# Performance work log

Hardware: AMD Instinct MI355X
Metric: run time of the kernel (lower is better)

The kernel has to match this reference:

```python
import math
import jax, jax.numpy as jnp
import numpy as np

NH, NKV, HD, THETA = 32, 8, 128, 500000.0

def rotate_half(x):
    x1, x2 = jnp.split(x, 2, axis=-1)
    return jnp.concatenate((-x2, x1), axis=-1)

def rope_cos_sin(seq_len, dim, base, dtype):
    inv_freq = 1.0 / (base ** (jnp.arange(0, dim, 2, dtype=jnp.float32) / dim))
    t = jnp.arange(seq_len, dtype=jnp.float32)
    freqs = jnp.outer(t, inv_freq)              # [S, dim/2]
    emb = jnp.concatenate((freqs, freqs), -1)   # [S, dim]
    return jnp.cos(emb).astype(dtype), jnp.sin(emb).astype(dtype)

def setup_inputs() -> dict:
    key = jax.random.key(0)
    ks = jax.random.split(key, 5)
    B, S, H = 1, 2048, 4096
    sc = 1.0 / math.sqrt(H)
    return {
        'x':  jax.random.normal(ks[0], (B, S, H), jnp.float32),
        'wq': jax.random.normal(ks[1], (H, H), jnp.float32) * sc,
        'wk': jax.random.normal(ks[2], (NKV * HD, H), jnp.float32) * sc,
        'wv': jax.random.normal(ks[3], (NKV * HD, H), jnp.float32) * sc,
        'wo': jax.random.normal(ks[4], (H, H), jnp.float32) * sc,
    }

def attention(x, wq, wk, wv, wo):
    B, S, H = x.shape
    n_rep = NH // NKV
    q = (x @ wq.T).reshape(B, S, NH, HD).transpose(0, 2, 1, 3)    # [B,NH,S,HD]
    k = (x @ wk.T).reshape(B, S, NKV, HD).transpose(0, 2, 1, 3)   # [B,NKV,S,HD]
    v = (x @ wv.T).reshape(B, S, NKV, HD).transpose(0, 2, 1, 3)
    cos, sin = rope_cos_sin(S, HD, THETA, x.dtype)                # [S,HD]
    cos = cos[None, None]; sin = sin[None, None]
    q = q * cos + rotate_half(q) * sin
    k = k * cos + rotate_half(k) * sin
    k = jnp.repeat(k, n_rep, axis=1)                               # [B,NH,S,HD]
    v = jnp.repeat(v, n_rep, axis=1)
    scores = jnp.einsum('bhqd,bhkd->bhqk', q, k) / math.sqrt(HD)
    causal = jnp.tril(jnp.ones((S, S), dtype=bool))
    scores = jnp.where(causal, scores, jnp.finfo(scores.dtype).min)
    probs = jax.nn.softmax(scores, axis=-1)
    out = jnp.einsum('bhqk,bhkd->bhqd', probs, v)                  # [B,NH,S,HD]
    out = out.transpose(0, 2, 1, 3).reshape(B, S, H)
    return out @ wo.T

def reference(x, wq, wk, wv, wo):
    return attention(x, wq, wk, wv, wo)
```

## Files before the change

### kernel.cpp

```cpp
#include <hip/hip_runtime.h>
#include <hip/hip_bf16.h>
#include <math.h>

typedef __bf16 bf16x8 __attribute__((ext_vector_type(8)));
typedef __bf16 bf16x4 __attribute__((ext_vector_type(4)));
typedef unsigned short u16x8 __attribute__((ext_vector_type(8)));
typedef float  f32x4  __attribute__((ext_vector_type(4)));

constexpr int kS   = 2048;
constexpr int kH   = 4096;
constexpr int kNH  = 32;
constexpr int kNKV = 8;
constexpr int kHD  = 128;
constexpr int kQKV = kH + 2 * kNKV * kHD;
constexpr int kKOff = kH;
constexpr int kVOff = kH + kNKV * kHD;

__global__ void cast_bf16(const float* __restrict__ in, __bf16* __restrict__ out, int n4) {
    int i = blockIdx.x * blockDim.x + threadIdx.x;
    if (i < n4) {
        float4 f = ((const float4*)in)[i];
        bf16x4 o;
        o[0] = (__bf16)f.x; o[1] = (__bf16)f.y; o[2] = (__bf16)f.z; o[3] = (__bf16)f.w;
        ((bf16x4*)out)[i] = o;
    }
}

__global__ void cast_all(const float* __restrict__ x, const float* __restrict__ wq,
                         const float* __restrict__ wk, const float* __restrict__ wv,
                         __bf16* __restrict__ xb, __bf16* __restrict__ wqkv) {
    int i = blockIdx.x * 256 + threadIdx.x;
    float4 f;
    __bf16* dst;
    int di;
    if (i < (1 << 21)) {
        f = ((const float4*)x)[i];
        dst = xb; di = i;
    } else {
        int j = i - (1 << 21);
        const float4* s = (j < (1 << 22)) ? ((const float4*)wq + j)
                        : (j < (5 << 20)) ? ((const float4*)wk + (j - (1 << 22)))
                                          : ((const float4*)wv + (j - (5 << 20)));
        f = *s;
        dst = wqkv; di = j;
    }
    bf16x4 o;
    o[0] = (__bf16)f.x; o[1] = (__bf16)f.y; o[2] = (__bf16)f.z; o[3] = (__bf16)f.w;
    ((bf16x4*)dst)[di] = o;
}

constexpr int BM = 128, BN = 128, BK = 32;

__device__ inline void gld16(const __bf16* g, __bf16* l) {
    __builtin_amdgcn_global_load_lds((const __attribute__((address_space(1))) void*)g,
                                     (__attribute__((address_space(3))) void*)l, 16, 0, 0);
}

template <typename OutT>
__global__ __launch_bounds__(256) void gemm_nt(const __bf16* __restrict__ A,
                                               const __bf16* __restrict__ B,
                                               OutT* __restrict__ C,
                                               int M, int N, int K) {
    __shared__ __align__(16) __bf16 As[BM * BK];
    __shared__ __align__(16) __bf16 Bs[BN * BK];
    const int tid  = threadIdx.x;
    const int w    = tid >> 6, lane = tid & 63;
    const int m0   = blockIdx.y * BM, n0 = blockIdx.x * BN;
    const int wm   = (w >> 1) * 64, wn = (w & 1) * 64;
    const int lr   = lane & 15, lk = (lane >> 4) * 8;

    const int ci0 = w * 128 + lane;
    const int ci1 = ci0 + 64;
    const __bf16* gA0 = A + (size_t)(m0 + (ci0 >> 2)) * K + (ci0 & 3) * 8;
    const __bf16* gA1 = A + (size_t)(m0 + (ci1 >> 2)) * K + (ci1 & 3) * 8;
    const __bf16* gB0 = B + (size_t)(n0 + (ci0 >> 2)) * K + (ci0 & 3) * 8;
    const __bf16* gB1 = B + (size_t)(n0 + (ci1 >> 2)) * K + (ci1 & 3) * 8;
    __bf16* lA0 = As + w * 1024;
    __bf16* lA1 = As + w * 1024 + 512;
    __bf16* lB0 = Bs + w * 1024;
    __bf16* lB1 = Bs + w * 1024 + 512;

    f32x4 acc[4][4];
#pragma unroll
    for (int i = 0; i < 4; i++)
#pragma unroll
        for (int j = 0; j < 4; j++) acc[i][j] = (f32x4)(0.f);

    for (int k0 = 0; k0 < K; k0 += BK) {
        gld16(gA0 + k0, lA0);
        gld16(gA1 + k0, lA1);
        gld16(gB0 + k0, lB0);
        gld16(gB1 + k0, lB1);
        __syncthreads();

        bf16x8 af[4], bfr[4];
#pragma unroll
        for (int i = 0; i < 4; i++) af[i]  = *(const bf16x8*)&As[(wm + i * 16 + lr) * BK + lk];
#pragma unroll
        for (int j = 0; j < 4; j++) bfr[j] = *(const bf16x8*)&Bs[(wn + j * 16 + lr) * BK + lk];

#pragma unroll
        for (int i = 0; i < 4; i++)
#pragma unroll
            for (int j = 0; j < 4; j++)
                acc[i][j] = __builtin_amdgcn_mfma_f32_16x16x32_bf16(af[i], bfr[j], acc[i][j], 0, 0, 0);
        __syncthreads();
    }

    const int cr = (lane >> 4) * 4, cc = lane & 15;
#pragma unroll
    for (int i = 0; i < 4; i++)
#pragma unroll
        for (int j = 0; j < 4; j++) {
            OutT* Cp = C + (size_t)(m0 + wm + i * 16 + cr) * N + (n0 + wn + j * 16 + cc);
#pragma unroll
            for (int r = 0; r < 4; r++) Cp[(size_t)r * N] = (OutT)acc[i][j][r];
        }
}

__global__ void rope_qkv(__bf16* __restrict__ qkv) {
    int idx  = blockIdx.x * 256 + threadIdx.x;
    int d    = idx & 63;
    int rest = idx >> 6;
    int hh   = rest % (kNH + kNKV);
    int s    = rest / (kNH + kNKV);
    float inv_freq = powf(500000.0f, -(float)d * (1.0f / 64.0f));
    float sn, cs;
    sincosf((float)s * inv_freq, &sn, &cs);
    __bf16* base = qkv + (size_t)s * kQKV + ((hh < kNH) ? hh * kHD : kKOff + (hh - kNH) * kHD);
    float sc = (hh < kNH) ? 0.088388347648318447f : 1.0f;
    float a = (float)base[d], b = (float)base[d + 64];
    base[d]      = (__bf16)((a * cs - b * sn) * sc);
    base[d + 64] = (__bf16)((b * cs + a * sn) * sc);
}

constexpr int KSP = 136;
constexpr int VTP = 72;
constexpr int PSP = 68;

__global__ __launch_bounds__(256) void flash_attn(const __bf16* __restrict__ qkv,
                                                  __bf16* __restrict__ ob) {
    __shared__ __align__(16) __bf16 Ks[64 * KSP];
    __shared__ __align__(16) __bf16 Vt[128 * VTP];
    __shared__ __align__(16) float  Ps[4 * 16 * PSP];

    const int tid  = threadIdx.x;
    const int wave = tid >> 6, lane = tid & 63;
    const int bx   = blockIdx.x;
    const int kvh  = bx & 7;
    const int qt   = 127 - (bx >> 3);
    const int h    = kvh * 4 + wave;
    const int r    = lane & 15, g = lane >> 4;
    const int qglob = qt * 16 + r;

    bf16x8 qfrag[4];
    const __bf16* qrow = qkv + (size_t)(qt * 16 + r) * kQKV + h * kHD + g * 8;
#pragma unroll
    for (int c = 0; c < 4; c++) qfrag[c] = *(const bf16x8*)(qrow + c * 32);

    f32x4 o[8];
#pragma unroll
    for (int dt = 0; dt < 8; dt++) o[dt] = (f32x4)(0.f);
    float mrow = -3.0e38f, lrow = 0.f;
    float* Pw = Ps + wave * 16 * PSP;

    const int nkt = qt / 4 + 1;
    const int krow = tid & 63, kcb = (tid >> 6) * 32;
    const __bf16* kbase = qkv + kKOff + kvh * kHD;
    const __bf16* vbase = qkv + kVOff + kvh * kHD;

    for (int kt = 0; kt < nkt; ++kt) {
        const __bf16* Kg = kbase + (size_t)(kt * 64 + krow) * kQKV + kcb;
        __bf16* Kl = Ks + krow * KSP + kcb;
#pragma unroll
        for (int i = 0; i < 4; i++) *(bf16x8*)(Kl + i * 8) = *(const bf16x8*)(Kg + i * 8);
#pragma unroll
        for (int i = 0; i < 2; i++) {
            int task = tid * 2 + i;
            int p = task & 31, c = task >> 5;
            const __bf16* v0 = vbase + (size_t)(kt * 64 + 2 * p) * kQKV + c * 8;
            u16x8 a = __builtin_bit_cast(u16x8, *(const bf16x8*)v0);
            u16x8 b = __builtin_bit_cast(u16x8, *(const bf16x8*)(v0 + kQKV));
#pragma unroll
            for (int j = 0; j < 8; j++) {
                unsigned int pk = (unsigned int)a[j] | ((unsigned int)b[j] << 16);
                *(unsigned int*)(Vt + (c * 8 + j) * VTP + 2 * p) = pk;
            }
        }
        __syncthreads();

        f32x4 st[4];
#pragma unroll
        for (int t = 0; t < 4; t++) st[t] = (f32x4)(0.f);
#pragma unroll
        for (int c = 0; c < 4; c++) {
#pragma unroll
            for (int t = 0; t < 4; t++) {
                bf16x8 kf = *(const bf16x8*)&Ks[(t * 16 + r) * KSP + c * 32 + g * 8];
                st[t] = __builtin_amdgcn_mfma_f32_16x16x32_bf16(kf, qfrag[c], st[t], 0, 0, 0);
            }
        }

        float mloc = -3.0e38f;
#pragma unroll
        for (int t = 0; t < 4; t++)
#pragma unroll
            for (int reg = 0; reg < 4; reg++) {
                int key = kt * 64 + t * 16 + g * 4 + reg;
                float v = (key <= qglob) ? st[t][reg] : -3.0e38f;
                st[t][reg] = v;
                mloc = fmaxf(mloc, v);
            }
        mloc = fmaxf(mloc, __shfl_xor(mloc, 16));
        mloc = fmaxf(mloc, __shfl_xor(mloc, 32));
        float mnew  = fmaxf(mrow, mloc);
        float alpha = __expf(mrow - mnew);
        mrow = mnew;
        float lsum = 0.f;
#pragma unroll
        for (int t = 0; t < 4; t++)
#pragma unroll
            for (int reg = 0; reg < 4; reg++) {
                float pv = __expf(st[t][reg] - mnew);
                st[t][reg] = pv;
                lsum += pv;
            }
        lsum += __shfl_xor(lsum, 16);
        lsum += __shfl_xor(lsum, 32);
        lrow = lrow * alpha + lsum;

        float ar[4];
#pragma unroll
        for (int reg = 0; reg < 4; reg++) ar[reg] = __shfl(alpha, g * 4 + reg);
#pragma unroll
        for (int dt = 0; dt < 8; dt++)
#pragma unroll
            for (int reg = 0; reg < 4; reg++) o[dt][reg] *= ar[reg];

#pragma unroll
        for (int t = 0; t < 4; t++)
            *(f32x4*)&Pw[r * PSP + t * 16 + g * 4] = st[t];
        __asm__ volatile("s_waitcnt lgkmcnt(0)" ::: "memory");

#pragma unroll
        for (int kc = 0; kc < 2; kc++) {
            f32x4 p0 = *(const f32x4*)&Pw[r * PSP + kc * 32 + g * 8];
            f32x4 p1 = *(const f32x4*)&Pw[r * PSP + kc * 32 + g * 8 + 4];
            bf16x8 pf;
#pragma unroll
            for (int j = 0; j < 4; j++) { pf[j] = (__bf16)p0[j]; pf[j + 4] = (__bf16)p1[j]; }
#pragma unroll
            for (int dt = 0; dt < 8; dt++) {
                bf16x8 vf = *(const bf16x8*)&Vt[(dt * 16 + r) * VTP + kc * 32 + g * 8];
                o[dt] = __builtin_amdgcn_mfma_f32_16x16x32_bf16(pf, vf, o[dt], 0, 0, 0);
            }
        }
        __syncthreads();
    }

    float linv = 1.f / lrow;
    float lr4[4];
#pragma unroll
    for (int reg = 0; reg < 4; reg++) lr4[reg] = __shfl(linv, g * 4 + reg);
#pragma unroll
    for (int dt = 0; dt < 8; dt++)
#pragma unroll
        for (int reg = 0; reg < 4; reg++) {
            int qq = g * 4 + reg, dd = dt * 16 + r;
            ob[(size_t)(qt * 16 + qq) * kH + h * kHD + dd] = (__bf16)(o[dt][reg] * lr4[reg]);
        }
}

extern "C" void kernel_launch(void* const* d_in, const int* in_sizes, int n_in,
                              void* d_out, int out_size, void* d_ws, size_t ws_size,
                              hipStream_t stream) {
    const float* x  = (const float*)d_in[0];
    const float* wq = (const float*)d_in[1];
    const float* wk = (const float*)d_in[2];
    const float* wv = (const float*)d_in[3];
    const float* wo = (const float*)d_in[4];
    float* out = (float*)d_out;

    char* p = (char*)d_ws;
    auto alloc = [&](size_t bytes) {
        char* r = p;
        p += (bytes + 255) & ~(size_t)255;
        return r;
    };
    __bf16* xb    = (__bf16*)alloc((size_t)kS * kH * 2);
    __bf16* wqkvb = (__bf16*)alloc((size_t)kQKV * kH * 2);
    __bf16* qkv   = (__bf16*)alloc((size_t)kS * kQKV * 2);
    __bf16* ao    = xb;
    __bf16* wob   = wqkvb;

    cast_all<<<dim3(1 << 15), 256, 0, stream>>>(x, wq, wk, wv, xb, wqkvb);

    gemm_nt<__bf16><<<dim3(kQKV / BN, kS / BM), 256, 0, stream>>>(xb, wqkvb, qkv, kS, kQKV, kH);

    rope_qkv<<<dim3(kS * (kNH + kNKV) * 64 / 256), 256, 0, stream>>>(qkv);

    cast_bf16<<<dim3((kH * kH / 4) / 256), 256, 0, stream>>>(wo, wob, kH * kH / 4);

    flash_attn<<<dim3(kNKV * (kS / 16)), 256, 0, stream>>>(qkv, ao);

    gemm_nt<float><<<dim3(kH / BN, kS / BM), 256, 0, stream>>>(ao, wob, out, kS, kH, kH);
}
```

Measured before the change: 564.6 us.

## Double GEMM K-tile to 64 with XOR-swizzled LDS layout

Raises the GEMM K-step from 32 to 64, halving the barrier and loop overhead per unit of K. Each wave now issues four direct-to-LDS 16-byte loads per operand. The LDS tile is XOR-swizzled by row so the wider rows avoid bank conflicts on fragment reads. LDS use per block doubles, which may reduce occupancy, and the loads are still not double-buffered.

```diff
diff --git a/kernel.cpp b/kernel.cpp
--- a/kernel.cpp
+++ b/kernel.cpp
@@ -49,7 +49,7 @@
     ((bf16x4*)dst)[di] = o;
 }
 
-constexpr int BM = 128, BN = 128, BK = 32;
+constexpr int BM = 128, BN = 128, BK = 64;
 
 __device__ inline void gld16(const __bf16* g, __bf16* l) {
     __builtin_amdgcn_global_load_lds((const __attribute__((address_space(1))) void*)g,
@@ -67,18 +67,20 @@
     const int w    = tid >> 6, lane = tid & 63;
     const int m0   = blockIdx.y * BM, n0 = blockIdx.x * BN;
     const int wm   = (w >> 1) * 64, wn = (w & 1) * 64;
-    const int lr   = lane & 15, lk = (lane >> 4) * 8;
-
-    const int ci0 = w * 128 + lane;
-    const int ci1 = ci0 + 64;
-    const __bf16* gA0 = A + (size_t)(m0 + (ci0 >> 2)) * K + (ci0 & 3) * 8;
-    const __bf16* gA1 = A + (size_t)(m0 + (ci1 >> 2)) * K + (ci1 & 3) * 8;
-    const __bf16* gB0 = B + (size_t)(n0 + (ci0 >> 2)) * K + (ci0 & 3) * 8;
-    const __bf16* gB1 = B + (size_t)(n0 + (ci1 >> 2)) * K + (ci1 & 3) * 8;
-    __bf16* lA0 = As + w * 1024;
-    __bf16* lA1 = As + w * 1024 + 512;
-    __bf16* lB0 = Bs + w * 1024;
-    __bf16* lB1 = Bs + w * 1024 + 512;
+    const int lr   = lane & 15, g8 = lane >> 4;
+
+    const int l3 = lane >> 3;
+    const int lc = (lane & 7) ^ l3;
+    const __bf16 *gA[4], *gB[4];
+    __bf16 *lA[4], *lB[4];
+#pragma unroll
+    for (int c = 0; c < 4; c++) {
+        int G = w * 4 + c;
+        gA[c] = A + (size_t)(m0 + G * 8 + l3) * K + lc * 8;
+        gB[c] = B + (size_t)(n0 + G * 8 + l3) * K + lc * 8;
+        lA[c] = As + G * 512;
+        lB[c] = Bs + G * 512;
+    }
 
     f32x4 acc[4][4];
 #pragma unroll
@@ -87,27 +89,33 @@
         for (int j = 0; j < 4; j++) acc[i][j] = (f32x4)(0.f);
 
     for (int k0 = 0; k0 < K; k0 += BK) {
-        gld16(gA0 + k0, lA0);
-        gld16(gA1 + k0, lA1);
-        gld16(gB0 + k0, lB0);
-        gld16(gB1 + k0, lB1);
+#pragma unroll
+        for (int c = 0; c < 4; c++) {
+            gld16(gA[c] + k0, lA[c]);
+            gld16(gB[c] + k0, lB[c]);
+        }
         __syncthreads();
 
-        bf16x8 af[4], bfr[4];
-#pragma unroll
-        for (int i = 0; i < 4; i++) af[i]  = *(const bf16x8*)&As[(wm + i * 16 + lr) * BK + lk];
-#pragma unroll
-        for (int j = 0; j < 4; j++) bfr[j] = *(const bf16x8*)&Bs[(wn + j * 16 + lr) * BK + lk];
-
-#pragma unroll
-        for (int i = 0; i < 4; i++)
+        const int rx = lr & 7;
+#pragma unroll
+        for (int kc = 0; kc < 2; kc++) {
+            bf16x8 af[4], bfr[4];
+#pragma unroll
+            for (int i = 0; i < 4; i++)
+                af[i]  = *(const bf16x8*)&As[(wm + i * 16 + lr) * BK + (((kc * 4 + g8) ^ rx) * 8)];
 #pragma unroll
             for (int j = 0; j < 4; j++)
-                acc[i][j] = __builtin_amdgcn_mfma_f32_16x16x32_bf16(af[i], bfr[j], acc[i][j], 0, 0, 0);
+                bfr[j] = *(const bf16x8*)&Bs[(wn + j * 16 + lr) * BK + (((kc * 4 + g8) ^ rx) * 8)];
+#pragma unroll
+            for (int i = 0; i < 4; i++)
+#pragma unroll
+                for (int j = 0; j < 4; j++)
+                    acc[i][j] = __builtin_amdgcn_mfma_f32_16x16x32_bf16(af[i], bfr[j], acc[i][j], 0, 0, 0);
+        }
         __syncthreads();
     }
 
-    const int cr = (lane >> 4) * 4, cc = lane & 15;
+    const int cr = g8 * 4, cc = lr;
 #pragma unroll
     for (int i = 0; i < 4; i++)
 #pragma unroll
```

Result: faster. 529.0 us (-6.3%).
